# Performance work log

Hardware: AMD Instinct MI355X
Metric: run time of the kernel (lower is better)

## Reference

```python
import jax, jax.numpy as jnp
import numpy as np

B, T, D, H = 8, 1024, 1024, 16
DH = D // H
EPS = 1e-5


def setup_inputs() -> dict:
    key = jax.random.key(0)
    ks = jax.random.split(key, 8)
    s = 0.02
    return {
        "x": jax.random.normal(ks[0], (B, T, D), dtype=jnp.float32),
        # per-head Q/K/V weights stacked: (H, in_c, d_head), applied as x @ W
        "Wq": jax.random.normal(ks[1], (H, D, DH), dtype=jnp.float32) * s,
        "Wk": jax.random.normal(ks[2], (H, D, DH), dtype=jnp.float32) * s,
        "Wv": jax.random.normal(ks[3], (H, D, DH), dtype=jnp.float32) * s,
        # FFN weights stored (in, out): y = x @ W
        "W1": jax.random.normal(ks[4], (D, D), dtype=jnp.float32) * s,
        "W2": jax.random.normal(ks[5], (D, D), dtype=jnp.float32) * s,
        "g1": jnp.ones((D,), jnp.float32),
        "b1": jnp.zeros((D,), jnp.float32),
        "g2": jnp.ones((D,), jnp.float32),
        "b2": jnp.zeros((D,), jnp.float32),
    }


def _layer_norm(x, g, b):
    m = jnp.mean(x, axis=-1, keepdims=True)
    v = jnp.mean((x - m) ** 2, axis=-1, keepdims=True)  # biased, as torch LN
    return (x - m) * jax.lax.rsqrt(v + EPS) * g + b


def reference(x, Wq, Wk, Wv, W1, W2, g1, b1, g2, b2):
    b, t, d = x.shape
    dh = Wq.shape[-1]
    q = jnp.einsum("btc,hcd->bhtd", x, Wq)
    k = jnp.einsum("btc,hcd->bhtd", x, Wk)
    v = jnp.einsum("btc,hcd->bhtd", x, Wv)
    attn = jnp.einsum("bhtd,bhsd->bhts", q, k) / (dh ** 0.5)
    # Original: attn @ ones(T,T) -> every column equals rowsum(attn);
    # softmax(dim=1) over the query axis is then constant across columns,
    # so out[t] = softmax_t(rowsum)[t] * sum_s v[s]. Same math, reduced.
    rowsum = attn.sum(axis=-1)               # (B,H,T)
    p = jax.nn.softmax(rowsum, axis=-1)      # softmax over query index t
    vsum = v.sum(axis=2)                     # (B,H,DH)
    head_out = p[..., None] * vsum[:, :, None, :]        # (B,H,T,DH)
    out = head_out.transpose(0, 2, 1, 3).reshape(b, t, d)  # concat heads
    x1 = _layer_norm(x + out, g1, b1)
    ff = jax.nn.relu(x1 @ W1) @ W2           # dropout = identity (eval)
    return _layer_norm(x1 + ff, g2, b2)
```

## Files before the change

kernel.cpp:

```cpp
#include <hip/hip_runtime.h>

#define NB 8
#define NT 1024
#define ND 1024
#define NH 16
#define NDH 64
#define NM (NB*NT)
#define LNEPS 1e-5f

typedef __attribute__((ext_vector_type(8))) __bf16 bf16x8;
typedef __attribute__((ext_vector_type(4))) float f32x4;

__global__ void transpose_to_bf16(const float* __restrict__ W1, const float* __restrict__ W2,
                                  __bf16* __restrict__ WT1, __bf16* __restrict__ WT2) {
    __shared__ float tile[32][33];
    const float* W = blockIdx.z ? W2 : W1;
    __bf16* WT = blockIdx.z ? WT2 : WT1;
    int bx = blockIdx.x * 32;
    int by = blockIdx.y * 32;
    int tx = threadIdx.x;
    int ty = threadIdx.y;
    for (int i = ty; i < 32; i += 8)
        tile[i][tx] = W[(size_t)(by + i) * ND + bx + tx];
    __syncthreads();
    for (int i = ty; i < 32; i += 8)
        WT[(size_t)(bx + i) * ND + by + tx] = (__bf16)tile[tx][i];
}

__global__ void xsum_kernel(const float* __restrict__ x, float* __restrict__ xsum) {
    int b = blockIdx.x;
    int chunk = blockIdx.y;
    int tid = threadIdx.x;
    const float4* xp = (const float4*)(x + ((size_t)b * NT + chunk * 16) * ND) + tid;
    float4 s = {0.f, 0.f, 0.f, 0.f};
    #pragma unroll
    for (int t = 0; t < 16; ++t) {
        float4 v = xp[(size_t)t * (ND / 4)];
        s.x += v.x; s.y += v.y; s.z += v.z; s.w += v.w;
    }
    float* dst = xsum + b * ND + tid * 4;
    atomicAdd(dst + 0, s.x);
    atomicAdd(dst + 1, s.y);
    atomicAdd(dst + 2, s.z);
    atomicAdd(dst + 3, s.w);
}

__global__ void head_prep(const float* __restrict__ xsum,
                          const float* __restrict__ Wq, const float* __restrict__ Wk,
                          const float* __restrict__ Wv,
                          float* __restrict__ vsum, float* __restrict__ wqk) {
    int h = blockIdx.x, b = blockIdx.y;
    int t = threadIdx.x;
    int d = t & 63, q = t >> 6;
    __shared__ float part[2][4][NDH];
    __shared__ float ks[NDH];
    const float* xs = xsum + b * ND;
    float sk = 0.f, sv = 0.f;
    for (int c = q * 256; c < q * 256 + 256; ++c) {
        float xv = xs[c];
        sk += xv * Wk[((size_t)h * ND + c) * NDH + d];
        sv += xv * Wv[((size_t)h * ND + c) * NDH + d];
    }
    part[0][q][d] = sk;
    part[1][q][d] = sv;
    __syncthreads();
    if (t < 64) {
        ks[t] = part[0][0][t] + part[0][1][t] + part[0][2][t] + part[0][3][t];
    } else if (t < 128) {
        int dd = t - 64;
        vsum[((size_t)b * NH + h) * NDH + dd] =
            part[1][0][dd] + part[1][1][dd] + part[1][2][dd] + part[1][3][dd];
    }
    __syncthreads();
    for (int c = t; c < ND; c += 256) {
        const float* wq = Wq + ((size_t)h * ND + c) * NDH;
        float s = 0.f;
        #pragma unroll 16
        for (int dd = 0; dd < NDH; ++dd) s += wq[dd] * ks[dd];
        wqk[((size_t)b * NH + h) * ND + c] = s * 0.125f;
    }
}

__global__ __launch_bounds__(256) void rowsum_kernel(const float* __restrict__ x,
                                                     const float* __restrict__ wqk,
                                                     float* __restrict__ rowsum) {
    __shared__ float wl[NH * ND];
    int tc = blockIdx.x, b = blockIdx.y;
    int tid = threadIdx.x, wid = tid >> 6, lane = tid & 63;
    {
        const float4* wsrc = (const float4*)(wqk + (size_t)b * NH * ND);
        float4* wdst = (float4*)wl;
        #pragma unroll
        for (int i = 0; i < 16; ++i) wdst[tid + i * 256] = wsrc[tid + i * 256];
    }
    __syncthreads();
    const float4* wl4 = (const float4*)wl;
    #pragma unroll
    for (int j = 0; j < 4; ++j) {
        int t = tc * 16 + wid * 4 + j;
        const float4* xrow = (const float4*)(x + ((size_t)b * NT + t) * ND);
        float4 xv[4];
        #pragma unroll
        for (int c = 0; c < 4; ++c) xv[c] = xrow[c * 64 + lane];
        #pragma unroll
        for (int h = 0; h < NH; ++h) {
            float p = 0.f;
            #pragma unroll
            for (int c = 0; c < 4; ++c) {
                float4 wv = wl4[h * 256 + c * 64 + lane];
                p += xv[c].x * wv.x + xv[c].y * wv.y + xv[c].z * wv.z + xv[c].w * wv.w;
            }
            for (int off = 32; off; off >>= 1) p += __shfl_down(p, off, 64);
            if (lane == 0) rowsum[((size_t)b * NH + h) * NT + t] = p;
        }
    }
}

__global__ void softmax_kernel(float* __restrict__ rs) {
    int bh = blockIdx.x, tid = threadIdx.x;
    int wave = tid >> 6, lane = tid & 63;
    float* row = rs + (size_t)bh * NT;
    float4 v = ((float4*)row)[tid];
    float m = fmaxf(fmaxf(v.x, v.y), fmaxf(v.z, v.w));
    __shared__ float red[4];
    for (int off = 32; off; off >>= 1) m = fmaxf(m, __shfl_down(m, off, 64));
    if (lane == 0) red[wave] = m;
    __syncthreads();
    m = fmaxf(fmaxf(red[0], red[1]), fmaxf(red[2], red[3]));
    __syncthreads();
    float4 e;
    e.x = __expf(v.x - m); e.y = __expf(v.y - m);
    e.z = __expf(v.z - m); e.w = __expf(v.w - m);
    float s = e.x + e.y + e.z + e.w;
    for (int off = 32; off; off >>= 1) s += __shfl_down(s, off, 64);
    if (lane == 0) red[wave] = s;
    __syncthreads();
    s = red[0] + red[1] + red[2] + red[3];
    float inv = 1.f / s;
    e.x *= inv; e.y *= inv; e.z *= inv; e.w *= inv;
    ((float4*)row)[tid] = e;
}

__global__ void ln1_kernel(const float* __restrict__ x, const float* __restrict__ p,
                           const float* __restrict__ vsum,
                           const float* __restrict__ g1, const float* __restrict__ b1,
                           __bf16* __restrict__ x1b) {
    int t = blockIdx.x, b = blockIdx.y, tid = threadIdx.x;
    int wave = tid >> 6, lane = tid & 63;
    size_t rowoff = ((size_t)b * NT + t) * ND;
    float4 xv = ((const float4*)(x + rowoff))[tid];
    int h = tid >> 4;
    float pv = p[((size_t)b * NH + h) * NT + t];
    float4 vs = ((const float4*)(vsum + ((size_t)b * NH + h) * NDH))[tid & 15];
    float4 s;
    s.x = xv.x + pv * vs.x; s.y = xv.y + pv * vs.y;
    s.z = xv.z + pv * vs.z; s.w = xv.w + pv * vs.w;
    float sum = s.x + s.y + s.z + s.w;
    float sq = s.x * s.x + s.y * s.y + s.z * s.z + s.w * s.w;
    __shared__ float rs_[4], rq_[4];
    for (int off = 32; off; off >>= 1) {
        sum += __shfl_down(sum, off, 64);
        sq += __shfl_down(sq, off, 64);
    }
    if (lane == 0) { rs_[wave] = sum; rq_[wave] = sq; }
    __syncthreads();
    sum = rs_[0] + rs_[1] + rs_[2] + rs_[3];
    sq = rq_[0] + rq_[1] + rq_[2] + rq_[3];
    float mu = sum * (1.f / ND);
    float var = sq * (1.f / ND) - mu * mu;
    float rstd = rsqrtf(var + LNEPS);
    float4 g = ((const float4*)g1)[tid];
    float4 bb = ((const float4*)b1)[tid];
    union { __bf16 h4[4]; uint2 u; } pk;
    pk.h4[0] = (__bf16)((s.x - mu) * rstd * g.x + bb.x);
    pk.h4[1] = (__bf16)((s.y - mu) * rstd * g.y + bb.y);
    pk.h4[2] = (__bf16)((s.z - mu) * rstd * g.z + bb.z);
    pk.h4[3] = (__bf16)((s.w - mu) * rstd * g.w + bb.w);
    ((uint2*)(x1b + rowoff))[tid] = pk.u;
}

template <int RELU>
__global__ __launch_bounds__(256) void gemm_bf16(const __bf16* __restrict__ A,
                                                 const __bf16* __restrict__ BT,
                                                 __bf16* __restrict__ Cout) {
    const int K = 1024, N = 1024;
    __shared__ __bf16 As[128][32];
    __shared__ __bf16 Bs[128][32];
    int raw = blockIdx.x;
    int swz = (raw & 7) * 64 + (raw >> 3);
    int m0 = (swz >> 3) * 128;
    int n0 = (swz & 7) * 128;
    int tid = threadIdx.x;
    int wid = tid >> 6, lane = tid & 63;
    int wr = wid >> 1, wc = wid & 1;
    int r = lane & 15, g = lane >> 4;
    int srow = wid * 32 + (lane >> 2);
    int skoff = (lane & 3) * 8;
    const __bf16* Ag = A + (size_t)(m0 + srow) * K + skoff;
    const __bf16* Bg = BT + (size_t)(n0 + srow) * K + skoff;
    f32x4 acc[4][4] = {};
    for (int k0 = 0; k0 < K; k0 += 32) {
        __syncthreads();
        __builtin_amdgcn_global_load_lds(
            (const __attribute__((address_space(1))) unsigned int*)(Ag + k0),
            (__attribute__((address_space(3))) unsigned int*)&As[wid * 32][0], 16, 0, 0);
        __builtin_amdgcn_global_load_lds(
            (const __attribute__((address_space(1))) unsigned int*)(Ag + (size_t)16 * K + k0),
            (__attribute__((address_space(3))) unsigned int*)&As[wid * 32 + 16][0], 16, 0, 0);
        __builtin_amdgcn_global_load_lds(
            (const __attribute__((address_space(1))) unsigned int*)(Bg + k0),
            (__attribute__((address_space(3))) unsigned int*)&Bs[wid * 32][0], 16, 0, 0);
        __builtin_amdgcn_global_load_lds(
            (const __attribute__((address_space(1))) unsigned int*)(Bg + (size_t)16 * K + k0),
            (__attribute__((address_space(3))) unsigned int*)&Bs[wid * 32 + 16][0], 16, 0, 0);
        __syncthreads();
        bf16x8 af[4], bf[4];
        #pragma unroll
        for (int mf = 0; mf < 4; ++mf)
            af[mf] = *(const bf16x8*)&As[wr * 64 + mf * 16 + r][g * 8];
        #pragma unroll
        for (int nf = 0; nf < 4; ++nf)
            bf[nf] = *(const bf16x8*)&Bs[wc * 64 + nf * 16 + r][g * 8];
        #pragma unroll
        for (int mf = 0; mf < 4; ++mf)
            #pragma unroll
            for (int nf = 0; nf < 4; ++nf)
                acc[mf][nf] = __builtin_amdgcn_mfma_f32_16x16x32_bf16(af[mf], bf[nf], acc[mf][nf], 0, 0, 0);
    }
    #pragma unroll
    for (int mf = 0; mf < 4; ++mf) {
        #pragma unroll
        for (int nf = 0; nf < 4; ++nf) {
            int col = n0 + wc * 64 + nf * 16 + r;
            #pragma unroll
            for (int i = 0; i < 4; ++i) {
                int row = m0 + wr * 64 + mf * 16 + g * 4 + i;
                float v = acc[mf][nf][i];
                if (RELU) v = fmaxf(v, 0.f);
                Cout[(size_t)row * N + col] = (__bf16)v;
            }
        }
    }
}

__global__ void ln2_kernel(const __bf16* __restrict__ x1b, const __bf16* __restrict__ ffb,
                           float* __restrict__ out,
                           const float* __restrict__ g2, const float* __restrict__ b2) {
    int t = blockIdx.x, b = blockIdx.y, tid = threadIdx.x;
    int wave = tid >> 6, lane = tid & 63;
    size_t rowoff = ((size_t)b * NT + t) * ND;
    union { __bf16 h4[4]; uint2 u; } pk, pf;
    pk.u = ((const uint2*)(x1b + rowoff))[tid];
    pf.u = ((const uint2*)(ffb + rowoff))[tid];
    float4 s;
    s.x = (float)pk.h4[0] + (float)pf.h4[0];
    s.y = (float)pk.h4[1] + (float)pf.h4[1];
    s.z = (float)pk.h4[2] + (float)pf.h4[2];
    s.w = (float)pk.h4[3] + (float)pf.h4[3];
    float sum = s.x + s.y + s.z + s.w;
    float sq = s.x * s.x + s.y * s.y + s.z * s.z + s.w * s.w;
    __shared__ float rs_[4], rq_[4];
    for (int off = 32; off; off >>= 1) {
        sum += __shfl_down(sum, off, 64);
        sq += __shfl_down(sq, off, 64);
    }
    if (lane == 0) { rs_[wave] = sum; rq_[wave] = sq; }
    __syncthreads();
    sum = rs_[0] + rs_[1] + rs_[2] + rs_[3];
    sq = rq_[0] + rq_[1] + rq_[2] + rq_[3];
    float mu = sum * (1.f / ND);
    float var = sq * (1.f / ND) - mu * mu;
    float rstd = rsqrtf(var + LNEPS);
    float4 g = ((const float4*)g2)[tid];
    float4 bb = ((const float4*)b2)[tid];
    float4 o;
    o.x = (s.x - mu) * rstd * g.x + bb.x;
    o.y = (s.y - mu) * rstd * g.y + bb.y;
    o.z = (s.z - mu) * rstd * g.z + bb.z;
    o.w = (s.w - mu) * rstd * g.w + bb.w;
    ((float4*)(out + rowoff))[tid] = o;
}

extern "C" void kernel_launch(void* const* d_in, const int* in_sizes, int n_in,
                              void* d_out, int out_size, void* d_ws, size_t ws_size,
                              hipStream_t stream) {
    const float* x  = (const float*)d_in[0];
    const float* Wq = (const float*)d_in[1];
    const float* Wk = (const float*)d_in[2];
    const float* Wv = (const float*)d_in[3];
    const float* W1 = (const float*)d_in[4];
    const float* W2 = (const float*)d_in[5];
    const float* g1 = (const float*)d_in[6];
    const float* b1 = (const float*)d_in[7];
    const float* g2 = (const float*)d_in[8];
    const float* b2 = (const float*)d_in[9];
    float* out = (float*)d_out;

    char* w = (char*)d_ws;
    float* xsum = (float*)w;   w += (size_t)NB * ND * 4;
    float* vsum = (float*)w;   w += (size_t)NB * NH * NDH * 4;
    float* wqk  = (float*)w;   w += (size_t)NB * NH * ND * 4;
    float* rsum = (float*)w;   w += (size_t)NB * NH * NT * 4;
    __bf16* x1b = (__bf16*)w;  w += (size_t)NM * ND * 2;
    __bf16* h1b = (__bf16*)w;  w += (size_t)NM * ND * 2;
    __bf16* ffb = (__bf16*)w;  w += (size_t)NM * ND * 2;
    __bf16* w1t = (__bf16*)w;  w += (size_t)ND * ND * 2;
    __bf16* w2t = (__bf16*)w;  w += (size_t)ND * ND * 2;

    hipMemsetAsync(xsum, 0, (size_t)NB * ND * 4, stream);

    transpose_to_bf16<<<dim3(32, 32, 2), dim3(32, 8), 0, stream>>>(W1, W2, w1t, w2t);

    xsum_kernel<<<dim3(NB, 64), 256, 0, stream>>>(x, xsum);
    head_prep<<<dim3(NH, NB), 256, 0, stream>>>(xsum, Wq, Wk, Wv, vsum, wqk);
    rowsum_kernel<<<dim3(64, NB), 256, 0, stream>>>(x, wqk, rsum);
    softmax_kernel<<<NB * NH, 256, 0, stream>>>(rsum);
    ln1_kernel<<<dim3(NT, NB), 256, 0, stream>>>(x, rsum, vsum, g1, b1, x1b);

    gemm_bf16<1><<<512, 256, 0, stream>>>(x1b, w1t, h1b);
    gemm_bf16<0><<<512, 256, 0, stream>>>(h1b, w2t, ffb);
    ln2_kernel<<<dim3(NT, NB), 256, 0, stream>>>(x1b, ffb, out, g2, b2);
}
```

Baseline: 235.7 us.

## Restructure rowsum kernel: drop LDS staging, register-block rows, butterfly reduce

The rowsum kernel no longer stages the 64KB per-batch wqk matrix in shared memory. Each wave now reads the weights straight from global memory and accumulates 4 rows times 16 heads in registers. The per-head shuffle reductions are replaced by a recursive-halving butterfly exchange that ends with lane h holding head h's sum, which is then written as a single float4. This removes the LDS fill, the block barrier and most shuffles, and lets the kernel run at higher occupancy. The cost is more register pressure and weight reads that now go through cache rather than shared memory.

```diff
diff --git a/kernel.cpp b/kernel.cpp
--- a/kernel.cpp
+++ b/kernel.cpp
@@ -84,35 +84,65 @@
 __global__ __launch_bounds__(256) void rowsum_kernel(const float* __restrict__ x,
                                                      const float* __restrict__ wqk,
                                                      float* __restrict__ rowsum) {
-    __shared__ float wl[NH * ND];
     int tc = blockIdx.x, b = blockIdx.y;
     int tid = threadIdx.x, wid = tid >> 6, lane = tid & 63;
-    {
-        const float4* wsrc = (const float4*)(wqk + (size_t)b * NH * ND);
-        float4* wdst = (float4*)wl;
-        #pragma unroll
-        for (int i = 0; i < 16; ++i) wdst[tid + i * 256] = wsrc[tid + i * 256];
-    }
-    __syncthreads();
-    const float4* wl4 = (const float4*)wl;
-    #pragma unroll
-    for (int j = 0; j < 4; ++j) {
-        int t = tc * 16 + wid * 4 + j;
-        const float4* xrow = (const float4*)(x + ((size_t)b * NT + t) * ND);
+    int t0 = tc * 16 + wid * 4;
+    float acc[4][16];
+    #pragma unroll
+    for (int tq = 0; tq < 4; ++tq)
+        #pragma unroll
+        for (int h = 0; h < 16; ++h) acc[tq][h] = 0.f;
+    const float4* wb = (const float4*)(wqk + (size_t)b * NH * ND);
+    #pragma unroll
+    for (int chunk = 0; chunk < 4; ++chunk) {
         float4 xv[4];
         #pragma unroll
-        for (int c = 0; c < 4; ++c) xv[c] = xrow[c * 64 + lane];
-        #pragma unroll
-        for (int h = 0; h < NH; ++h) {
-            float p = 0.f;
+        for (int tq = 0; tq < 4; ++tq)
+            xv[tq] = ((const float4*)(x + ((size_t)b * NT + t0 + tq) * ND))[chunk * 64 + lane];
+        #pragma unroll
+        for (int h = 0; h < 16; ++h) {
+            float4 wv = wb[h * 256 + chunk * 64 + lane];
             #pragma unroll
-            for (int c = 0; c < 4; ++c) {
-                float4 wv = wl4[h * 256 + c * 64 + lane];
-                p += xv[c].x * wv.x + xv[c].y * wv.y + xv[c].z * wv.z + xv[c].w * wv.w;
-            }
-            for (int off = 32; off; off >>= 1) p += __shfl_down(p, off, 64);
-            if (lane == 0) rowsum[((size_t)b * NH + h) * NT + t] = p;
-        }
+            for (int tq = 0; tq < 4; ++tq)
+                acc[tq][h] += xv[tq].x * wv.x + xv[tq].y * wv.y +
+                              xv[tq].z * wv.z + xv[tq].w * wv.w;
+        }
+    }
+    bool c0 = lane & 1, c1 = lane & 2, c2 = lane & 4, c3 = lane & 8;
+    float out4[4];
+    #pragma unroll
+    for (int tq = 0; tq < 4; ++tq) {
+        float w8[8];
+        #pragma unroll
+        for (int j = 0; j < 8; ++j) {
+            float send = c0 ? acc[tq][2 * j] : acc[tq][2 * j + 1];
+            float recv = __shfl_xor(send, 1, 64);
+            w8[j] = (c0 ? acc[tq][2 * j + 1] : acc[tq][2 * j]) + recv;
+        }
+        float u4[4];
+        #pragma unroll
+        for (int j = 0; j < 4; ++j) {
+            float send = c1 ? w8[2 * j] : w8[2 * j + 1];
+            float recv = __shfl_xor(send, 2, 64);
+            u4[j] = (c1 ? w8[2 * j + 1] : w8[2 * j]) + recv;
+        }
+        float s2[2];
+        #pragma unroll
+        for (int j = 0; j < 2; ++j) {
+            float send = c2 ? u4[2 * j] : u4[2 * j + 1];
+            float recv = __shfl_xor(send, 4, 64);
+            s2[j] = (c2 ? u4[2 * j + 1] : u4[2 * j]) + recv;
+        }
+        float send = c3 ? s2[0] : s2[1];
+        float recv = __shfl_xor(send, 8, 64);
+        float r = (c3 ? s2[1] : s2[0]) + recv;
+        r += __shfl_xor(r, 16, 64);
+        r += __shfl_xor(r, 32, 64);
+        out4[tq] = r;
+    }
+    if (lane < 16) {
+        float4 o = {out4[0], out4[1], out4[2], out4[3]};
+        *(float4*)(rowsum + ((size_t)b * NH + lane) * NT + t0) = o;
     }
 }
 
```

After: 232.8 us. No clear change (-1.2%).
